# Kernel optimization log

Hardware: AMD Instinct MI355X
Metric: run time of the kernel (lower is better)

## Reference

```python
import jax, jax.numpy as jnp
import numpy as np

T, D_IN, D_OUT, E = 8192, 1024, 1024, 8
LN_EPS = 1e-5


def setup_inputs() -> dict:
    key = jax.random.key(0)
    k1, k2, k3 = jax.random.split(key, 3)
    x = jax.random.normal(k1, (T, D_IN), dtype=jnp.float32)
    # tokens are pre-sorted by expert; equal load => capacity = T // E per expert
    expert_frequency = jnp.full((E,), T // E, dtype=jnp.int64)
    # per-expert Linear(input_dim, output_dim) params
    W = jax.random.normal(k2, (E, D_IN, D_OUT), dtype=jnp.float32) / np.sqrt(D_IN)
    b = jax.random.normal(k3, (E, D_OUT), dtype=jnp.float32) * 0.02
    # per-expert LayerNorm(output_dim) affine params
    ln_gamma = jnp.ones((E, D_OUT), dtype=jnp.float32)
    ln_beta = jnp.zeros((E, D_OUT), dtype=jnp.float32)
    return {
        "expert_ordered_input": x,
        "expert_frequency": expert_frequency,
        "W": W,
        "b": b,
        "ln_gamma": ln_gamma,
        "ln_beta": ln_beta,
    }


def reference(expert_ordered_input, expert_frequency, W, b, ln_gamma, ln_beta):
    # Grouped-GEMM form of: split tokens by expert_frequency, apply per-expert
    # LayerBlock (Linear -> relu -> LayerNorm), then concat along token dim.
    # Frequencies are equal (capacity = T // E), so the ragged split is a reshape.
    x = expert_ordered_input
    n_tok, d_in = x.shape
    n_exp = W.shape[0]
    cap = n_tok // n_exp  # static capacity per expert
    xe = x.reshape(n_exp, cap, d_in)                       # [E, cap, d_in]
    h = jnp.einsum("ecd,edf->ecf", xe, W) + b[:, None, :]  # [E, cap, d_out]
    h = jax.nn.relu(h)
    mu = jnp.mean(h, axis=-1, keepdims=True)
    var = jnp.var(h, axis=-1, keepdims=True)
    hn = (h - mu) * jax.lax.rsqrt(var + LN_EPS)
    out = hn * ln_gamma[:, None, :] + ln_beta[:, None, :]
    return out.reshape(n_tok, -1)                          # concat over experts
```

## Files before the change

kernel.cpp:

```cpp
#include <hip/hip_runtime.h>
#include <hip/hip_bf16.h>
#include <stdint.h>

#define T_TOK 8192
#define DIN   1024
#define DOUT  1024
#define NEXP  8
#define CAP   1024
#define LN_EPS 1e-5f

#define BM 128
#define BN 128
#define BK 32
#define LDSS 48

typedef __attribute__((ext_vector_type(8))) short short8;
typedef __attribute__((ext_vector_type(4))) float f32x4;

__device__ __forceinline__ unsigned short f2bf(float f) {
    union { float f; unsigned int u; } v; v.f = f;
    unsigned int u = v.u;
    unsigned int r = u + 0x7FFFu + ((u >> 16) & 1u);
    return (unsigned short)(r >> 16);
}
__device__ __forceinline__ float bf2f(unsigned short h) {
    union { unsigned int u; float f; } v; v.u = ((unsigned int)h) << 16;
    return v.f;
}

__device__ __forceinline__ void gld16(void* l, const void* g) {
    __builtin_amdgcn_global_load_lds(
        (const __attribute__((address_space(1))) unsigned int*)(uintptr_t)g,
        (__attribute__((address_space(3))) unsigned int*)(uintptr_t)l,
        16, 0, 0);
}

__global__ __launch_bounds__(256) void prep_kernel(
    const float* __restrict__ X, const float* __restrict__ W,
    unsigned short* __restrict__ Xb, unsigned short* __restrict__ Wt) {
    __shared__ float tile[32][33];
    int blk = blockIdx.x;
    int tid = threadIdx.x;
    if (blk < 8192) {
        int i = blk * 256 + tid;
        float4 v = ((const float4*)X)[i];
        ushort4 o;
        o.x = f2bf(v.x); o.y = f2bf(v.y); o.z = f2bf(v.z); o.w = f2bf(v.w);
        ((ushort4*)Xb)[i] = o;
    } else {
        int t  = blk - 8192;
        int e  = t >> 10;
        int k0 = ((t >> 5) & 31) * 32;
        int n0 = (t & 31) * 32;
        const float* Wp = W + (size_t)e * DIN * DOUT;
        unsigned short* Wtp = Wt + (size_t)e * DIN * DOUT;
        {
            int k  = tid >> 3;
            int c4 = tid & 7;
            float4 v = *(const float4*)(Wp + (size_t)(k0 + k) * DOUT + n0 + c4 * 4);
            tile[k][c4 * 4 + 0] = v.x; tile[k][c4 * 4 + 1] = v.y;
            tile[k][c4 * 4 + 2] = v.z; tile[k][c4 * 4 + 3] = v.w;
        }
        __syncthreads();
        {
            int n  = tid >> 3;
            int kc = tid & 7;
            ushort4 o;
            o.x = f2bf(tile[kc * 4 + 0][n]);
            o.y = f2bf(tile[kc * 4 + 1][n]);
            o.z = f2bf(tile[kc * 4 + 2][n]);
            o.w = f2bf(tile[kc * 4 + 3][n]);
            *(ushort4*)(Wtp + (size_t)(n0 + n) * DIN + k0 + kc * 4) = o;
        }
    }
}

__global__ __launch_bounds__(256, 2) void gemm4_kernel(
    const unsigned short* __restrict__ Xb,
    const unsigned short* __restrict__ Wt,
    const float* __restrict__ Bias,
    unsigned short* __restrict__ Hb,
    float2* __restrict__ P)
{
    __shared__ unsigned short As[BM * BK];
    __shared__ unsigned short Bs[BN * BK];

    int blk = blockIdx.x;
    int e   = blk & 7;
    int mi  = blk >> 6;
    int m0  = mi * BM;
    int ni  = (blk >> 3) & 7;
    int n0  = ni * BN;

    int tid  = threadIdx.x;
    int wave = tid >> 6;
    int lane = tid & 63;
    int wm   = (wave >> 1) * 64;
    int wn   = (wave & 1) * 64;
    int lrow = lane & 15;
    int quad = lane >> 4;

    const unsigned short* Ag = Xb + (size_t)(e * CAP + m0) * DIN;
    const unsigned short* Bg = Wt + (size_t)e * DOUT * DIN + (size_t)n0 * DIN;

    int l0 = tid;
    int l1 = tid + 256;
    int ar0 = l0 >> 2, ac0 = (l0 & 3) * 8;
    int ar1 = l1 >> 2, ac1 = (l1 & 3) * 8;

    f32x4 acc[4][4];
#pragma unroll
    for (int i = 0; i < 4; i++)
#pragma unroll
        for (int j = 0; j < 4; j++)
            acc[i][j] = (f32x4)(0.0f);

    for (int k0 = 0; k0 < DIN; k0 += BK) {
        gld16(&As[l0 * 8], Ag + (size_t)ar0 * DIN + k0 + ac0);
        gld16(&As[l1 * 8], Ag + (size_t)ar1 * DIN + k0 + ac1);
        gld16(&Bs[l0 * 8], Bg + (size_t)ar0 * DIN + k0 + ac0);
        gld16(&Bs[l1 * 8], Bg + (size_t)ar1 * DIN + k0 + ac1);
        __syncthreads();

        short8 af[4], bf[4];
#pragma unroll
        for (int i = 0; i < 4; i++)
            af[i] = *(const short8*)&As[(wm + i * 16 + lrow) * BK + quad * 8];
#pragma unroll
        for (int j = 0; j < 4; j++)
            bf[j] = *(const short8*)&Bs[(wn + j * 16 + lrow) * BK + quad * 8];
#pragma unroll
        for (int i = 0; i < 4; i++)
#pragma unroll
            for (int j = 0; j < 4; j++)
                acc[i][j] = __builtin_amdgcn_mfma_f32_16x16x32_bf16(af[i], bf[j], acc[i][j], 0, 0, 0);
        __syncthreads();
    }

    float bias[4];
#pragma unroll
    for (int j = 0; j < 4; j++)
        bias[j] = Bias[e * DOUT + n0 + wn + j * 16 + lrow];

    int tok0  = e * CAP + m0 + wm;
    int chunk = ni * 2 + (wave & 1);

#pragma unroll
    for (int i = 0; i < 4; i++) {
#pragma unroll
        for (int r = 0; r < 4; r++) {
            float s = 0.f, ss = 0.f;
#pragma unroll
            for (int j = 0; j < 4; j++) {
                float v = fmaxf(acc[i][j][r] + bias[j], 0.f);
                acc[i][j][r] = v;
                s += v;
                ss = fmaf(v, v, ss);
            }
#pragma unroll
            for (int m = 1; m <= 8; m <<= 1) {
                s  += __shfl_xor(s, m);
                ss += __shfl_xor(ss, m);
            }
            int grow = tok0 + i * 16 + quad * 4 + r;
            if (lrow == 0)
                P[(size_t)grow * 16 + chunk] = make_float2(s, ss);
#pragma unroll
            for (int j = 0; j < 4; j++) {
                int gcol = n0 + wn + j * 16 + lrow;
                Hb[(size_t)grow * DOUT + gcol] = f2bf(acc[i][j][r]);
            }
        }
    }
}

__global__ __launch_bounds__(256) void ln2_kernel(
    const unsigned short* __restrict__ Hb,
    const float2* __restrict__ P,
    const float* __restrict__ G,
    const float* __restrict__ Bt,
    float* __restrict__ Out)
{
    int row = blockIdx.x;
    int e   = row >> 10;
    int tid = threadIdx.x;
    __shared__ float sh[2];

    if (tid < 16) {
        float2 p = P[(size_t)row * 16 + tid];
        float s = p.x, ss = p.y;
#pragma unroll
        for (int m = 1; m <= 8; m <<= 1) {
            s  += __shfl_xor(s, m);
            ss += __shfl_xor(ss, m);
        }
        if (tid == 0) {
            float mu  = s * (1.0f / DOUT);
            float var = fmaxf(ss * (1.0f / DOUT) - mu * mu, 0.f);
            sh[0] = mu;
            sh[1] = rsqrtf(var + LN_EPS);
        }
    }
    __syncthreads();
    float mu = sh[0], rs = sh[1];

    ushort4 hb = ((const ushort4*)Hb)[(size_t)row * 256 + tid];
    float4 g = ((const float4*)G)[e * 256 + tid];
    float4 b = ((const float4*)Bt)[e * 256 + tid];
    float4 y;
    y.x = (bf2f(hb.x) - mu) * rs * g.x + b.x;
    y.y = (bf2f(hb.y) - mu) * rs * g.y + b.y;
    y.z = (bf2f(hb.z) - mu) * rs * g.z + b.z;
    y.w = (bf2f(hb.w) - mu) * rs * g.w + b.w;
    ((float4*)Out)[(size_t)row * 256 + tid] = y;
}

__global__ __launch_bounds__(256) void wt_only_kernel(const float* __restrict__ W,
                                                      unsigned short* __restrict__ Wt) {
    __shared__ float tile[32][33];
    int t  = blockIdx.x;
    int e  = t >> 10;
    int k0 = ((t >> 5) & 31) * 32;
    int n0 = (t & 31) * 32;
    int tid = threadIdx.x;
    const float* Wp = W + (size_t)e * DIN * DOUT;
    unsigned short* Wtp = Wt + (size_t)e * DIN * DOUT;
    {
        int k  = tid >> 3;
        int c4 = tid & 7;
        float4 v = *(const float4*)(Wp + (size_t)(k0 + k) * DOUT + n0 + c4 * 4);
        tile[k][c4 * 4 + 0] = v.x; tile[k][c4 * 4 + 1] = v.y;
        tile[k][c4 * 4 + 2] = v.z; tile[k][c4 * 4 + 3] = v.w;
    }
    __syncthreads();
    {
        int n  = tid >> 3;
        int kc = tid & 7;
        ushort4 o;
        o.x = f2bf(tile[kc * 4 + 0][n]);
        o.y = f2bf(tile[kc * 4 + 1][n]);
        o.z = f2bf(tile[kc * 4 + 2][n]);
        o.w = f2bf(tile[kc * 4 + 3][n]);
        *(ushort4*)(Wtp + (size_t)(n0 + n) * DIN + k0 + kc * 4) = o;
    }
}

__global__ __launch_bounds__(256, 2) void gemm_fb_kernel(
    const float* __restrict__ X, const unsigned short* __restrict__ Wt,
    const float* __restrict__ Bias, float* __restrict__ H)
{
    __shared__ unsigned short As[BM * LDSS];
    __shared__ unsigned short Bs[BN * LDSS];
    int blk = blockIdx.x;
    int e   = blk >> 6;
    int tt  = blk & 63;
    int m0  = (tt >> 3) * BM;
    int n0  = (tt & 7) * BN;
    int tid  = threadIdx.x;
    int wave = tid >> 6;
    int lane = tid & 63;
    int wm   = (wave >> 1) * 64;
    int wn   = (wave & 1) * 64;
    int lrow = lane & 15;
    int quad = lane >> 4;
    const float* Xe = X + (size_t)(e * CAP + m0) * DIN;
    const unsigned short* We = Wt + (size_t)e * DOUT * DIN + (size_t)n0 * DIN;
    f32x4 acc[4][4];
#pragma unroll
    for (int i = 0; i < 4; i++)
#pragma unroll
        for (int j = 0; j < 4; j++)
            acc[i][j] = (f32x4)(0.0f);
    for (int k0 = 0; k0 < DIN; k0 += BK) {
#pragma unroll
        for (int i = 0; i < 4; i++) {
            int idx = tid + i * 256;
            int row = idx >> 3;
            int c4  = idx & 7;
            const float4 xv = *(const float4*)(Xe + (size_t)row * DIN + k0 + c4 * 4);
            ushort4 bv;
            bv.x = f2bf(xv.x); bv.y = f2bf(xv.y); bv.z = f2bf(xv.z); bv.w = f2bf(xv.w);
            *(ushort4*)&As[row * LDSS + c4 * 4] = bv;
        }
#pragma unroll
        for (int i = 0; i < 2; i++) {
            int idx = tid + i * 256;
            int row = idx >> 2;
            int c   = idx & 3;
            uint4 wv = *(const uint4*)(We + (size_t)row * DIN + k0 + c * 8);
            *(uint4*)&Bs[row * LDSS + c * 8] = wv;
        }
        __syncthreads();
        short8 af[4], bf[4];
#pragma unroll
        for (int i = 0; i < 4; i++)
            af[i] = *(const short8*)&As[(wm + i * 16 + lrow) * LDSS + quad * 8];
#pragma unroll
        for (int j = 0; j < 4; j++)
            bf[j] = *(const short8*)&Bs[(wn + j * 16 + lrow) * LDSS + quad * 8];
#pragma unroll
        for (int i = 0; i < 4; i++)
#pragma unroll
            for (int j = 0; j < 4; j++)
                acc[i][j] = __builtin_amdgcn_mfma_f32_16x16x32_bf16(af[i], bf[j], acc[i][j], 0, 0, 0);
        __syncthreads();
    }
    float bias[4];
#pragma unroll
    for (int j = 0; j < 4; j++)
        bias[j] = Bias[e * DOUT + n0 + wn + j * 16 + lrow];
    int tok0 = e * CAP + m0 + wm;
#pragma unroll
    for (int i = 0; i < 4; i++)
#pragma unroll
        for (int j = 0; j < 4; j++) {
            int col = n0 + wn + j * 16 + lrow;
#pragma unroll
            for (int r = 0; r < 4; r++) {
                int row = tok0 + i * 16 + quad * 4 + r;
                float v = acc[i][j][r] + bias[j];
                H[(size_t)row * DOUT + col] = fmaxf(v, 0.0f);
            }
        }
}

__global__ __launch_bounds__(256) void ln_kernel(float* __restrict__ H,
                                                 const float* __restrict__ G,
                                                 const float* __restrict__ Bt) {
    int row = blockIdx.x;
    int e   = row >> 10;
    int tid  = threadIdx.x;
    int wave = tid >> 6;
    int lane = tid & 63;
    float* hp = H + (size_t)row * DOUT;
    float4 x = *(const float4*)(hp + tid * 4);
    float s  = x.x + x.y + x.z + x.w;
    float ss = fmaf(x.x, x.x, fmaf(x.y, x.y, fmaf(x.z, x.z, x.w * x.w)));
#pragma unroll
    for (int m = 32; m >= 1; m >>= 1) {
        s  += __shfl_xor(s, m);
        ss += __shfl_xor(ss, m);
    }
    __shared__ float red[8];
    if (lane == 0) { red[wave] = s; red[4 + wave] = ss; }
    __syncthreads();
    float ts  = red[0] + red[1] + red[2] + red[3];
    float tss = red[4] + red[5] + red[6] + red[7];
    float mean = ts * (1.0f / DOUT);
    float var  = fmaxf(tss * (1.0f / DOUT) - mean * mean, 0.0f);
    float rs = rsqrtf(var + LN_EPS);
    float4 g = *(const float4*)(G  + (size_t)e * DOUT + tid * 4);
    float4 b = *(const float4*)(Bt + (size_t)e * DOUT + tid * 4);
    float4 y;
    y.x = (x.x - mean) * rs * g.x + b.x;
    y.y = (x.y - mean) * rs * g.y + b.y;
    y.z = (x.z - mean) * rs * g.z + b.z;
    y.w = (x.w - mean) * rs * g.w + b.w;
    *(float4*)(hp + tid * 4) = y;
}

extern "C" void kernel_launch(void* const* d_in, const int* in_sizes, int n_in,
                              void* d_out, int out_size, void* d_ws, size_t ws_size,
                              hipStream_t stream) {
    const float* x  = (const float*)d_in[0];
    const float* W  = (const float*)d_in[2];
    const float* b  = (const float*)d_in[3];
    const float* g  = (const float*)d_in[4];
    const float* be = (const float*)d_in[5];
    float* out = (float*)d_out;

    const size_t WT_BYTES = (size_t)NEXP * DIN * DOUT * 2;
    const size_t XB_BYTES = (size_t)T_TOK * DIN * 2;
    const size_t HB_BYTES = (size_t)T_TOK * DOUT * 2;
    const size_t P_BYTES  = (size_t)T_TOK * 16 * 8;
    const size_t NEEDED   = WT_BYTES + XB_BYTES + HB_BYTES + P_BYTES;

    unsigned short* Wt = (unsigned short*)d_ws;
    dim3 tb(256);

    if (ws_size >= NEEDED) {
        unsigned short* Xb = (unsigned short*)((char*)d_ws + WT_BYTES);
        unsigned short* Hb = (unsigned short*)((char*)d_ws + WT_BYTES + XB_BYTES);
        float2* P = (float2*)((char*)d_ws + WT_BYTES + XB_BYTES + HB_BYTES);
        prep_kernel<<<dim3(16384), tb, 0, stream>>>(x, W, Xb, Wt);
        gemm4_kernel<<<dim3(512), tb, 0, stream>>>(Xb, Wt, b, Hb, P);
        ln2_kernel<<<dim3(8192), tb, 0, stream>>>(Hb, P, g, be, out);
    } else {
        wt_only_kernel<<<dim3(8192), tb, 0, stream>>>(W, Wt);
        gemm_fb_kernel<<<dim3(512), tb, 0, stream>>>(x, Wt, b, out);
        ln_kernel<<<dim3(8192), tb, 0, stream>>>(out, g, be);
    }
}
```

Baseline: 154.9 us.

## Fuse prep, GEMM and LayerNorm into one cooperative persistent kernel

```diff
diff --git a/kernel.cpp b/kernel.cpp
--- a/kernel.cpp
+++ b/kernel.cpp
@@ -1,6 +1,9 @@
 #include <hip/hip_runtime.h>
 #include <hip/hip_bf16.h>
+#include <hip/hip_cooperative_groups.h>
 #include <stdint.h>
+
+namespace cg = cooperative_groups;
 
 #define T_TOK 8192
 #define DIN   1024
@@ -12,7 +15,6 @@
 #define BM 128
 #define BN 128
 #define BK 32
-#define LDSS 48
 
 typedef __attribute__((ext_vector_type(8))) short short8;
 typedef __attribute__((ext_vector_type(4))) float f32x4;
@@ -33,6 +35,183 @@
         (const __attribute__((address_space(1))) unsigned int*)(uintptr_t)g,
         (__attribute__((address_space(3))) unsigned int*)(uintptr_t)l,
         16, 0, 0);
+}
+
+__global__ __launch_bounds__(256, 2) void fused_kernel(
+    const float* __restrict__ X,
+    const float* __restrict__ W,
+    const float* __restrict__ Bias,
+    const float* __restrict__ G,
+    const float* __restrict__ Bt,
+    unsigned short* __restrict__ Xb,
+    unsigned short* __restrict__ Wt,
+    float2* __restrict__ P,
+    float* __restrict__ Out)
+{
+    __shared__ __align__(16) char smem[16384];
+    unsigned short* As = (unsigned short*)smem;
+    unsigned short* Bs = (unsigned short*)(smem + 8192);
+    float (*tile)[33] = (float(*)[33])smem;
+
+    int blk = blockIdx.x;
+    int tid = threadIdx.x;
+    int e   = blk & 7;
+    int sub = blk >> 3;
+
+    {
+        const float4* Xe4 = (const float4*)(X + (size_t)e * CAP * DIN);
+        ushort4* Xb4 = (ushort4*)(Xb + (size_t)e * CAP * DIN);
+#pragma unroll
+        for (int it = 0; it < 16; it++) {
+            int i = sub * 4096 + it * 256 + tid;
+            float4 v = Xe4[i];
+            ushort4 o;
+            o.x = f2bf(v.x); o.y = f2bf(v.y); o.z = f2bf(v.z); o.w = f2bf(v.w);
+            Xb4[i] = o;
+        }
+    }
+    {
+        const float* Wp = W + (size_t)e * DIN * DOUT;
+        unsigned short* Wtp = Wt + (size_t)e * DIN * DOUT;
+        for (int it = 0; it < 16; it++) {
+            int t  = sub * 16 + it;
+            int k0 = (t >> 5) * 32;
+            int n0 = (t & 31) * 32;
+            {
+                int k  = tid >> 3;
+                int c4 = tid & 7;
+                float4 v = *(const float4*)(Wp + (size_t)(k0 + k) * DOUT + n0 + c4 * 4);
+                tile[k][c4 * 4 + 0] = v.x; tile[k][c4 * 4 + 1] = v.y;
+                tile[k][c4 * 4 + 2] = v.z; tile[k][c4 * 4 + 3] = v.w;
+            }
+            __syncthreads();
+            {
+                int n  = tid >> 3;
+                int kc = tid & 7;
+                ushort4 o;
+                o.x = f2bf(tile[kc * 4 + 0][n]);
+                o.y = f2bf(tile[kc * 4 + 1][n]);
+                o.z = f2bf(tile[kc * 4 + 2][n]);
+                o.w = f2bf(tile[kc * 4 + 3][n]);
+                *(ushort4*)(Wtp + (size_t)(n0 + n) * DIN + k0 + kc * 4) = o;
+            }
+            __syncthreads();
+        }
+    }
+
+    __threadfence();
+    cg::this_grid().sync();
+
+    int mi  = blk >> 6;
+    int m0  = mi * BM;
+    int ni  = (blk >> 3) & 7;
+    int n0  = ni * BN;
+
+    int wave = tid >> 6;
+    int lane = tid & 63;
+    int wm   = (wave >> 1) * 64;
+    int wn   = (wave & 1) * 64;
+    int lrow = lane & 15;
+    int quad = lane >> 4;
+
+    const unsigned short* Ag = Xb + (size_t)(e * CAP + m0) * DIN;
+    const unsigned short* Bg = Wt + (size_t)e * DOUT * DIN + (size_t)n0 * DIN;
+
+    int l0 = tid;
+    int l1 = tid + 256;
+    int ar0 = l0 >> 2, ac0 = (l0 & 3) * 8;
+    int ar1 = l1 >> 2, ac1 = (l1 & 3) * 8;
+
+    f32x4 acc[4][4];
+#pragma unroll
+    for (int i = 0; i < 4; i++)
+#pragma unroll
+        for (int j = 0; j < 4; j++)
+            acc[i][j] = (f32x4)(0.0f);
+
+    for (int k0 = 0; k0 < DIN; k0 += BK) {
+        gld16(&As[l0 * 8], Ag + (size_t)ar0 * DIN + k0 + ac0);
+        gld16(&As[l1 * 8], Ag + (size_t)ar1 * DIN + k0 + ac1);
+        gld16(&Bs[l0 * 8], Bg + (size_t)ar0 * DIN + k0 + ac0);
+        gld16(&Bs[l1 * 8], Bg + (size_t)ar1 * DIN + k0 + ac1);
+        __syncthreads();
+
+        short8 af[4], bf[4];
+#pragma unroll
+        for (int i = 0; i < 4; i++)
+            af[i] = *(const short8*)&As[(wm + i * 16 + lrow) * BK + quad * 8];
+#pragma unroll
+        for (int j = 0; j < 4; j++)
+            bf[j] = *(const short8*)&Bs[(wn + j * 16 + lrow) * BK + quad * 8];
+#pragma unroll
+        for (int i = 0; i < 4; i++)
+#pragma unroll
+            for (int j = 0; j < 4; j++)
+                acc[i][j] = __builtin_amdgcn_mfma_f32_16x16x32_bf16(af[i], bf[j], acc[i][j], 0, 0, 0);
+        __syncthreads();
+    }
+
+    float bias[4], gg[4], bb[4];
+#pragma unroll
+    for (int j = 0; j < 4; j++) {
+        int col = e * DOUT + n0 + wn + j * 16 + lrow;
+        bias[j] = Bias[col];
+        gg[j]   = G[col];
+        bb[j]   = Bt[col];
+    }
+
+    int tok0  = e * CAP + m0 + wm;
+    int chunk = ni * 2 + (wave & 1);
+
+#pragma unroll
+    for (int i = 0; i < 4; i++) {
+#pragma unroll
+        for (int r = 0; r < 4; r++) {
+            float s = 0.f, ss = 0.f;
+#pragma unroll
+            for (int j = 0; j < 4; j++) {
+                float v = fmaxf(acc[i][j][r] + bias[j], 0.f);
+                acc[i][j][r] = v;
+                s += v;
+                ss = fmaf(v, v, ss);
+            }
+#pragma unroll
+            for (int m = 1; m <= 8; m <<= 1) {
+                s  += __shfl_xor(s, m);
+                ss += __shfl_xor(ss, m);
+            }
+            if (lrow == 0) {
+                int grow = tok0 + i * 16 + quad * 4 + r;
+                P[(size_t)grow * 16 + chunk] = make_float2(s, ss);
+            }
+        }
+    }
+
+    __threadfence();
+    cg::this_grid().sync();
+
+#pragma unroll
+    for (int i = 0; i < 4; i++) {
+#pragma unroll
+        for (int r = 0; r < 4; r++) {
+            int grow = tok0 + i * 16 + quad * 4 + r;
+            float2 pc = P[(size_t)grow * 16 + lrow];
+            float s = pc.x, ss = pc.y;
+#pragma unroll
+            for (int m = 1; m <= 8; m <<= 1) {
+                s  += __shfl_xor(s, m);
+                ss += __shfl_xor(ss, m);
+            }
+            float mu  = s * (1.0f / DOUT);
+            float var = fmaxf(ss * (1.0f / DOUT) - mu * mu, 0.f);
+            float rs  = rsqrtf(var + LN_EPS);
+#pragma unroll
+            for (int j = 0; j < 4; j++) {
+                int gcol = n0 + wn + j * 16 + lrow;
+                Out[(size_t)grow * DOUT + gcol] = (acc[i][j][r] - mu) * rs * gg[j] + bb[j];
+            }
+        }
+    }
 }
 
 __global__ __launch_bounds__(256) void prep_kernel(
@@ -84,14 +263,12 @@
 {
     __shared__ unsigned short As[BM * BK];
     __shared__ unsigned short Bs[BN * BK];
-
     int blk = blockIdx.x;
     int e   = blk & 7;
     int mi  = blk >> 6;
     int m0  = mi * BM;
     int ni  = (blk >> 3) & 7;
     int n0  = ni * BN;
-
     int tid  = threadIdx.x;
     int wave = tid >> 6;
     int lane = tid & 63;
@@ -99,29 +276,24 @@
     int wn   = (wave & 1) * 64;
     int lrow = lane & 15;
     int quad = lane >> 4;
-
     const unsigned short* Ag = Xb + (size_t)(e * CAP + m0) * DIN;
     const unsigned short* Bg = Wt + (size_t)e * DOUT * DIN + (size_t)n0 * DIN;
-
     int l0 = tid;
     int l1 = tid + 256;
     int ar0 = l0 >> 2, ac0 = (l0 & 3) * 8;
     int ar1 = l1 >> 2, ac1 = (l1 & 3) * 8;
-
     f32x4 acc[4][4];
 #pragma unroll
     for (int i = 0; i < 4; i++)
 #pragma unroll
         for (int j = 0; j < 4; j++)
             acc[i][j] = (f32x4)(0.0f);
-
     for (int k0 = 0; k0 < DIN; k0 += BK) {
         gld16(&As[l0 * 8], Ag + (size_t)ar0 * DIN + k0 + ac0);
         gld16(&As[l1 * 8], Ag + (size_t)ar1 * DIN + k0 + ac1);
         gld16(&Bs[l0 * 8], Bg + (size_t)ar0 * DIN + k0 + ac0);
         gld16(&Bs[l1 * 8], Bg + (size_t)ar1 * DIN + k0 + ac1);
         __syncthreads();
-
         short8 af[4], bf[4];
 #pragma unroll
         for (int i = 0; i < 4; i++)
@@ -136,15 +308,12 @@
                 acc[i][j] = __builtin_amdgcn_mfma_f32_16x16x32_bf16(af[i], bf[j], acc[i][j], 0, 0, 0);
         __syncthreads();
     }
-
     float bias[4];
 #pragma unroll
     for (int j = 0; j < 4; j++)
         bias[j] = Bias[e * DOUT + n0 + wn + j * 16 + lrow];
-
     int tok0  = e * CAP + m0 + wm;
     int chunk = ni * 2 + (wave & 1);
-
 #pragma unroll
     for (int i = 0; i < 4; i++) {
 #pragma unroll
@@ -185,7 +354,6 @@
     int e   = row >> 10;
     int tid = threadIdx.x;
     __shared__ float sh[2];
-
     if (tid < 16) {
         float2 p = P[(size_t)row * 16 + tid];
         float s = p.x, ss = p.y;
@@ -203,7 +371,6 @@
     }
     __syncthreads();
     float mu = sh[0], rs = sh[1];
-
     ushort4 hb = ((const ushort4*)Hb)[(size_t)row * 256 + tid];
     float4 g = ((const float4*)G)[e * 256 + tid];
     float4 b = ((const float4*)Bt)[e * 256 + tid];
@@ -215,150 +382,6 @@
     ((float4*)Out)[(size_t)row * 256 + tid] = y;
 }
 
-__global__ __launch_bounds__(256) void wt_only_kernel(const float* __restrict__ W,
-                                                      unsigned short* __restrict__ Wt) {
-    __shared__ float tile[32][33];
-    int t  = blockIdx.x;
-    int e  = t >> 10;
-    int k0 = ((t >> 5) & 31) * 32;
-    int n0 = (t & 31) * 32;
-    int tid = threadIdx.x;
-    const float* Wp = W + (size_t)e * DIN * DOUT;
-    unsigned short* Wtp = Wt + (size_t)e * DIN * DOUT;
-    {
-        int k  = tid >> 3;
-        int c4 = tid & 7;
-        float4 v = *(const float4*)(Wp + (size_t)(k0 + k) * DOUT + n0 + c4 * 4);
-        tile[k][c4 * 4 + 0] = v.x; tile[k][c4 * 4 + 1] = v.y;
-        tile[k][c4 * 4 + 2] = v.z; tile[k][c4 * 4 + 3] = v.w;
-    }
-    __syncthreads();
-    {
-        int n  = tid >> 3;
-        int kc = tid & 7;
-        ushort4 o;
-        o.x = f2bf(tile[kc * 4 + 0][n]);
-        o.y = f2bf(tile[kc * 4 + 1][n]);
-        o.z = f2bf(tile[kc * 4 + 2][n]);
-        o.w = f2bf(tile[kc * 4 + 3][n]);
-        *(ushort4*)(Wtp + (size_t)(n0 + n) * DIN + k0 + kc * 4) = o;
-    }
-}
-
-__global__ __launch_bounds__(256, 2) void gemm_fb_kernel(
-    const float* __restrict__ X, const unsigned short* __restrict__ Wt,
-    const float* __restrict__ Bias, float* __restrict__ H)
-{
-    __shared__ unsigned short As[BM * LDSS];
-    __shared__ unsigned short Bs[BN * LDSS];
-    int blk = blockIdx.x;
-    int e   = blk >> 6;
-    int tt  = blk & 63;
-    int m0  = (tt >> 3) * BM;
-    int n0  = (tt & 7) * BN;
-    int tid  = threadIdx.x;
-    int wave = tid >> 6;
-    int lane = tid & 63;
-    int wm   = (wave >> 1) * 64;
-    int wn   = (wave & 1) * 64;
-    int lrow = lane & 15;
-    int quad = lane >> 4;
-    const float* Xe = X + (size_t)(e * CAP + m0) * DIN;
-    const unsigned short* We = Wt + (size_t)e * DOUT * DIN + (size_t)n0 * DIN;
-    f32x4 acc[4][4];
-#pragma unroll
-    for (int i = 0; i < 4; i++)
-#pragma unroll
-        for (int j = 0; j < 4; j++)
-            acc[i][j] = (f32x4)(0.0f);
-    for (int k0 = 0; k0 < DIN; k0 += BK) {
-#pragma unroll
-        for (int i = 0; i < 4; i++) {
-            int idx = tid + i * 256;
-            int row = idx >> 3;
-            int c4  = idx & 7;
-            const float4 xv = *(const float4*)(Xe + (size_t)row * DIN + k0 + c4 * 4);
-            ushort4 bv;
-            bv.x = f2bf(xv.x); bv.y = f2bf(xv.y); bv.z = f2bf(xv.z); bv.w = f2bf(xv.w);
-            *(ushort4*)&As[row * LDSS + c4 * 4] = bv;
-        }
-#pragma unroll
-        for (int i = 0; i < 2; i++) {
-            int idx = tid + i * 256;
-            int row = idx >> 2;
-            int c   = idx & 3;
-            uint4 wv = *(const uint4*)(We + (size_t)row * DIN + k0 + c * 8);
-            *(uint4*)&Bs[row * LDSS + c * 8] = wv;
-        }
-        __syncthreads();
-        short8 af[4], bf[4];
-#pragma unroll
-        for (int i = 0; i < 4; i++)
-            af[i] = *(const short8*)&As[(wm + i * 16 + lrow) * LDSS + quad * 8];
-#pragma unroll
-        for (int j = 0; j < 4; j++)
-            bf[j] = *(const short8*)&Bs[(wn + j * 16 + lrow) * LDSS + quad * 8];
-#pragma unroll
-        for (int i = 0; i < 4; i++)
-#pragma unroll
-            for (int j = 0; j < 4; j++)
-                acc[i][j] = __builtin_amdgcn_mfma_f32_16x16x32_bf16(af[i], bf[j], acc[i][j], 0, 0, 0);
-        __syncthreads();
-    }
-    float bias[4];
-#pragma unroll
-    for (int j = 0; j < 4; j++)
-        bias[j] = Bias[e * DOUT + n0 + wn + j * 16 + lrow];
-    int tok0 = e * CAP + m0 + wm;
-#pragma unroll
-    for (int i = 0; i < 4; i++)
-#pragma unroll
-        for (int j = 0; j < 4; j++) {
-            int col = n0 + wn + j * 16 + lrow;
-#pragma unroll
-            for (int r = 0; r < 4; r++) {
-                int row = tok0 + i * 16 + quad * 4 + r;
-                float v = acc[i][j][r] + bias[j];
-                H[(size_t)row * DOUT + col] = fmaxf(v, 0.0f);
-            }
-        }
-}
-
-__global__ __launch_bounds__(256) void ln_kernel(float* __restrict__ H,
-                                                 const float* __restrict__ G,
-                                                 const float* __restrict__ Bt) {
-    int row = blockIdx.x;
-    int e   = row >> 10;
-    int tid  = threadIdx.x;
-    int wave = tid >> 6;
-    int lane = tid & 63;
-    float* hp = H + (size_t)row * DOUT;
-    float4 x = *(const float4*)(hp + tid * 4);
-    float s  = x.x + x.y + x.z + x.w;
-    float ss = fmaf(x.x, x.x, fmaf(x.y, x.y, fmaf(x.z, x.z, x.w * x.w)));
-#pragma unroll
-    for (int m = 32; m >= 1; m >>= 1) {
-        s  += __shfl_xor(s, m);
-        ss += __shfl_xor(ss, m);
-    }
-    __shared__ float red[8];
-    if (lane == 0) { red[wave] = s; red[4 + wave] = ss; }
-    __syncthreads();
-    float ts  = red[0] + red[1] + red[2] + red[3];
-    float tss = red[4] + red[5] + red[6] + red[7];
-    float mean = ts * (1.0f / DOUT);
-    float var  = fmaxf(tss * (1.0f / DOUT) - mean * mean, 0.0f);
-    float rs = rsqrtf(var + LN_EPS);
-    float4 g = *(const float4*)(G  + (size_t)e * DOUT + tid * 4);
-    float4 b = *(const float4*)(Bt + (size_t)e * DOUT + tid * 4);
-    float4 y;
-    y.x = (x.x - mean) * rs * g.x + b.x;
-    y.y = (x.y - mean) * rs * g.y + b.y;
-    y.z = (x.z - mean) * rs * g.z + b.z;
-    y.w = (x.w - mean) * rs * g.w + b.w;
-    *(float4*)(hp + tid * 4) = y;
-}
-
 extern "C" void kernel_launch(void* const* d_in, const int* in_sizes, int n_in,
                               void* d_out, int out_size, void* d_ws, size_t ws_size,
                               hipStream_t stream) {
@@ -371,23 +394,26 @@
 
     const size_t WT_BYTES = (size_t)NEXP * DIN * DOUT * 2;
     const size_t XB_BYTES = (size_t)T_TOK * DIN * 2;
+    const size_t P_BYTES  = (size_t)T_TOK * 16 * 8;
     const size_t HB_BYTES = (size_t)T_TOK * DOUT * 2;
-    const size_t P_BYTES  = (size_t)T_TOK * 16 * 8;
-    const size_t NEEDED   = WT_BYTES + XB_BYTES + HB_BYTES + P_BYTES;
 
     unsigned short* Wt = (unsigned short*)d_ws;
+    unsigned short* Xb = (unsigned short*)((char*)d_ws + WT_BYTES);
+    float2* P = (float2*)((char*)d_ws + WT_BYTES + XB_BYTES);
+    unsigned short* Hb = (unsigned short*)((char*)d_ws + WT_BYTES + XB_BYTES + P_BYTES);
+
     dim3 tb(256);
-
-    if (ws_size >= NEEDED) {
-        unsigned short* Xb = (unsigned short*)((char*)d_ws + WT_BYTES);
-        unsigned short* Hb = (unsigned short*)((char*)d_ws + WT_BYTES + XB_BYTES);
-        float2* P = (float2*)((char*)d_ws + WT_BYTES + XB_BYTES + HB_BYTES);
+    bool coop_ok = false;
+    if (ws_size >= WT_BYTES + XB_BYTES + P_BYTES) {
+        void* args[] = {(void*)&x, (void*)&W, (void*)&b, (void*)&g, (void*)&be,
+                        (void*)&Xb, (void*)&Wt, (void*)&P, (void*)&out};
+        hipError_t err = hipLaunchCooperativeKernel((const void*)fused_kernel,
+                                                    dim3(512), tb, args, 0, stream);
+        coop_ok = (err == hipSuccess);
+    }
+    if (!coop_ok && ws_size >= WT_BYTES + XB_BYTES + P_BYTES + HB_BYTES) {
         prep_kernel<<<dim3(16384), tb, 0, stream>>>(x, W, Xb, Wt);
         gemm4_kernel<<<dim3(512), tb, 0, stream>>>(Xb, Wt, b, Hb, P);
         ln2_kernel<<<dim3(8192), tb, 0, stream>>>(Hb, P, g, be, out);
-    } else {
-        wt_only_kernel<<<dim3(8192), tb, 0, stream>>>(W, Wt);
-        gemm_fb_kernel<<<dim3(512), tb, 0, stream>>>(x, Wt, b, out);
-        ln_kernel<<<dim3(8192), tb, 0, stream>>>(out, g, be);
-    }
-}
+    }
+}
```

Measured after the change: 390.3 us. 152% more time.
